# Kernel tuning notes

Hardware: AMD Instinct MI355X
Metric: run time of the kernel (lower is better)

The kernel has to match this reference:

```python
import jax, jax.numpy as jnp
import numpy as np

N_NEURONS = 50000   # dense_shape[0]
N_INPUT = 17400     # dense_shape[1] (LGN units)
NNZ = 1_000_000     # number of sparse synapses
B, T = 1, 256       # batch, timesteps
BKG_SPIKE_RATE = 4  # hardcoded in original call()


def setup_inputs() -> dict:
    key = jax.random.key(0)
    k1, k2, k3, k4, k5 = jax.random.split(key, 5)
    rows = jax.random.randint(k1, (NNZ,), 0, N_NEURONS, dtype=jnp.int32)
    cols = jax.random.randint(k2, (NNZ,), 0, N_INPUT, dtype=jnp.int32)
    weights = jax.random.normal(k3, (NNZ,), dtype=jnp.float32)
    bkg_weights = jax.random.normal(k4, (N_NEURONS,), dtype=jnp.float32)
    inp = jax.random.uniform(k5, (B, T, N_INPUT), dtype=jnp.float32)
    return {"inp": inp, "weights": weights, "bkg_weights": bkg_weights,
            "rows": rows, "cols": cols}


def reference(inp, weights, bkg_weights, rows, cols):
    b, t, n_in = inp.shape
    x = inp.reshape(b * t, n_in)                     # (BT, n_input)
    # Sparse COO matmul: current[n, bt] = sum_{k: rows[k]==n} weights[k] * x[bt, cols[k]]
    # Equivalent to tf.sparse.sparse_dense_matmul(W_sparse, x, adjoint_b=True).
    contrib = weights[:, None] * x.T[cols]           # (nnz, BT)
    cur = jax.ops.segment_sum(contrib, rows, num_segments=N_NEURONS)  # (N, BT)
    cur = cur.T                                      # (BT, N) -- tf.transpose
    # Background noise: uniform(0,1) < 1 is always True, so rest == BKG_SPIKE_RATE.
    u = jax.random.uniform(jax.random.key(42), (b, t, BKG_SPIKE_RATE))
    rest = jnp.sum((u < 1.0).astype(inp.dtype), axis=-1)   # (b, t), constant 4
    noise = bkg_weights[None, None, :] * rest[..., None]   # (b, t, N)
    return cur.reshape(b, t, -1) + noise
```

## Files before the change

### kernel.cpp

```cpp
#include <hip/hip_runtime.h>

#define N_NEURONS 50000
#define N_INPUT   17400
#define NNZ_TOTAL 1000000
#define T_STEPS   256
#define ELL_CAP   64

__global__ __launch_bounds__(256) void transpose_kernel(
    const float* __restrict__ inp, ushort* __restrict__ xTb) {
    __shared__ float tile[32][33];
    const int bx = blockIdx.x;
    const int by = blockIdx.y;
    const int tx = threadIdx.x;
    const int ty = threadIdx.y;

    const int c = bx * 32 + tx;
#pragma unroll
    for (int i = 0; i < 4; ++i) {
        const int r = by * 32 + ty + i * 8;
        if (c < N_INPUT)
            tile[ty + i * 8][tx] = inp[r * N_INPUT + c];
    }
    __syncthreads();

    const int t = by * 32 + tx;
#pragma unroll
    for (int i = 0; i < 4; ++i) {
        const int rr = bx * 32 + ty + i * 8;
        if (rr < N_INPUT) {
            unsigned u = __float_as_uint(tile[tx][ty + i * 8]);
            u += 0x7fffu + ((u >> 16) & 1u);
            xTb[(size_t)rr * T_STEPS + t] = (ushort)(u >> 16);
        }
    }
}

__global__ __launch_bounds__(256) void ell_build_kernel(
    const int* __restrict__ rows, const int* __restrict__ cols,
    const float* __restrict__ w, int* __restrict__ cnt,
    float2* __restrict__ ell) {
    const int i = blockIdx.x * blockDim.x + threadIdx.x;
    if (i < NNZ_TOTAL) {
        const int r = rows[i];
        const int p = atomicAdd(&cnt[r], 1);
        if (p < ELL_CAP)
            ell[(size_t)r * ELL_CAP + p] =
                make_float2(w[i], __int_as_float(cols[i]));
    }
}

__global__ __launch_bounds__(256) void spmm_kernel(
    const uint2* __restrict__ xT2,
    const int* __restrict__ cnt, const float2* __restrict__ ell,
    const float* __restrict__ bkg, float* __restrict__ out) {
    __shared__ float lds[16][260];
    const int tid  = threadIdx.x;
    const int lane = tid & 63;
    const int wv   = tid >> 6;
    const int base = blockIdx.x * 16;
    const int n0   = base + wv * 4;

    const int4   cv  = *(const int4*)&cnt[n0];
    const float4 bgv = *(const float4*)&bkg[n0];
    const int cs[4] = {min(cv.x, ELL_CAP), min(cv.y, ELL_CAP),
                       min(cv.z, ELL_CAP), min(cv.w, ELL_CAP)};
    float2 mv[4];
#pragma unroll
    for (int q = 0; q < 4; ++q)
        mv[q] = ell[(size_t)(n0 + q) * ELL_CAP + lane];

#pragma unroll
    for (int q = 0; q < 4; ++q) {
        float4 acc = make_float4(0.f, 0.f, 0.f, 0.f);
        const int c = cs[q];
        for (int k = 0; k < c; ++k) {
            const float wk = __shfl(mv[q].x, k);
            const int   ck = __float_as_int(__shfl(mv[q].y, k));
            const uint2 xv = xT2[(size_t)ck * 64 + lane];
            const float x0 = __uint_as_float((xv.x & 0xffffu) << 16);
            const float x1 = __uint_as_float(xv.x & 0xffff0000u);
            const float x2 = __uint_as_float((xv.y & 0xffffu) << 16);
            const float x3 = __uint_as_float(xv.y & 0xffff0000u);
            acc.x = fmaf(wk, x0, acc.x);
            acc.y = fmaf(wk, x1, acc.y);
            acc.z = fmaf(wk, x2, acc.z);
            acc.w = fmaf(wk, x3, acc.w);
        }
        const float b4 = 4.0f * ((q == 0) ? bgv.x : (q == 1) ? bgv.y
                                : (q == 2) ? bgv.z : bgv.w);
        acc.x += b4; acc.y += b4; acc.z += b4; acc.w += b4;
        *(float4*)&lds[wv * 4 + q][lane * 4] = acc;
    }
    __syncthreads();

    const int c4 = (tid & 3) * 4;
    const int t0 = tid >> 2;
#pragma unroll
    for (int t = t0; t < T_STEPS; t += 64) {
        float4 v;
        v.x = lds[c4 + 0][t];
        v.y = lds[c4 + 1][t];
        v.z = lds[c4 + 2][t];
        v.w = lds[c4 + 3][t];
        *(float4*)&out[(size_t)t * N_NEURONS + base + c4] = v;
    }
}

extern "C" void kernel_launch(void* const* d_in, const int* in_sizes, int n_in,
                              void* d_out, int out_size, void* d_ws,
                              size_t ws_size, hipStream_t stream) {
    const float* inp     = (const float*)d_in[0];
    const float* weights = (const float*)d_in[1];
    const float* bkg     = (const float*)d_in[2];
    const int*   rows    = (const int*)d_in[3];
    const int*   cols    = (const int*)d_in[4];
    float*       out     = (float*)d_out;

    size_t off = 0;
    auto wsalloc = [&](size_t bytes) -> void* {
        void* p = (char*)d_ws + off;
        off += (bytes + 255) & ~size_t(255);
        return p;
    };
    ushort* xTb = (ushort*)wsalloc(sizeof(ushort) * N_INPUT * T_STEPS);
    int*    cnt = (int*)wsalloc(sizeof(int) * N_NEURONS);
    float2* ell = (float2*)wsalloc(sizeof(float2) * N_NEURONS * ELL_CAP);
    (void)ws_size;

    hipMemsetAsync(cnt, 0, sizeof(int) * N_NEURONS, stream);

    transpose_kernel<<<dim3((N_INPUT + 31) / 32, T_STEPS / 32), dim3(32, 8), 0,
                       stream>>>(inp, xTb);

    const int nb = (NNZ_TOTAL + 255) / 256;
    ell_build_kernel<<<nb, 256, 0, stream>>>(rows, cols, weights, cnt, ell);

    spmm_kernel<<<N_NEURONS / 16, 256, 0, stream>>>(
        (const uint2*)xTb, cnt, ell, bkg, out);
}
```

Before: 229.5 us.

## Pack ELL entries into 32-bit words and batch gathers eight at a time

Each ELL entry now fits in one 32-bit word, with the column index in the high 16 bits and a bf16-rounded weight in the low 16 bits. This halves ELL storage and traffic. The SpMM inner loop issues eight independent gathers before doing the FMAs, which gives more memory-level parallelism. The count is rounded up to a multiple of eight, so the padded slots must read as zero; for that the memset now clears the whole ELL buffer, adding about 12.8MB of extra zeroing. Output uses nontemporal stores, and the bf16 weights reduce precision.

Result: faster. 201.4 us (-12.2%).

```diff
diff --git a/kernel.cpp b/kernel.cpp
--- a/kernel.cpp
+++ b/kernel.cpp
@@ -5,6 +5,8 @@
 #define NNZ_TOTAL 1000000
 #define T_STEPS   256
 #define ELL_CAP   64
+
+typedef float f4_t __attribute__((ext_vector_type(4)));
 
 __global__ __launch_bounds__(256) void transpose_kernel(
     const float* __restrict__ inp, ushort* __restrict__ xTb) {
@@ -38,20 +40,23 @@
 __global__ __launch_bounds__(256) void ell_build_kernel(
     const int* __restrict__ rows, const int* __restrict__ cols,
     const float* __restrict__ w, int* __restrict__ cnt,
-    float2* __restrict__ ell) {
+    unsigned* __restrict__ ell) {
     const int i = blockIdx.x * blockDim.x + threadIdx.x;
     if (i < NNZ_TOTAL) {
         const int r = rows[i];
         const int p = atomicAdd(&cnt[r], 1);
-        if (p < ELL_CAP)
+        if (p < ELL_CAP) {
+            unsigned u = __float_as_uint(w[i]);
+            u += 0x7fffu + ((u >> 16) & 1u);
             ell[(size_t)r * ELL_CAP + p] =
-                make_float2(w[i], __int_as_float(cols[i]));
+                ((unsigned)cols[i] << 16) | (u >> 16);
+        }
     }
 }
 
 __global__ __launch_bounds__(256) void spmm_kernel(
     const uint2* __restrict__ xT2,
-    const int* __restrict__ cnt, const float2* __restrict__ ell,
+    const int* __restrict__ cnt, const unsigned* __restrict__ ell,
     const float* __restrict__ bkg, float* __restrict__ out) {
     __shared__ float lds[16][260];
     const int tid  = threadIdx.x;
@@ -62,32 +67,37 @@
 
     const int4   cv  = *(const int4*)&cnt[n0];
     const float4 bgv = *(const float4*)&bkg[n0];
-    const int cs[4] = {min(cv.x, ELL_CAP), min(cv.y, ELL_CAP),
-                       min(cv.z, ELL_CAP), min(cv.w, ELL_CAP)};
-    float2 mv[4];
+    unsigned ev[4];
 #pragma unroll
     for (int q = 0; q < 4; ++q)
-        mv[q] = ell[(size_t)(n0 + q) * ELL_CAP + lane];
+        ev[q] = ell[(size_t)(n0 + q) * ELL_CAP + lane];
 
 #pragma unroll
     for (int q = 0; q < 4; ++q) {
+        const int c = min((q == 0) ? cv.x : (q == 1) ? cv.y
+                          : (q == 2) ? cv.z : cv.w, ELL_CAP);
+        const int cpad = (c + 7) & ~7;
         float4 acc = make_float4(0.f, 0.f, 0.f, 0.f);
-        const int c = cs[q];
-        for (int k = 0; k < c; ++k) {
-            const float wk = __shfl(mv[q].x, k);
-            const int   ck = __float_as_int(__shfl(mv[q].y, k));
-            const uint2 xv = xT2[(size_t)ck * 64 + lane];
-            const float x0 = __uint_as_float((xv.x & 0xffffu) << 16);
-            const float x1 = __uint_as_float(xv.x & 0xffff0000u);
-            const float x2 = __uint_as_float((xv.y & 0xffffu) << 16);
-            const float x3 = __uint_as_float(xv.y & 0xffff0000u);
-            acc.x = fmaf(wk, x0, acc.x);
-            acc.y = fmaf(wk, x1, acc.y);
-            acc.z = fmaf(wk, x2, acc.z);
-            acc.w = fmaf(wk, x3, acc.w);
+
+        for (int k0 = 0; k0 < cpad; k0 += 8) {
+            unsigned e[8];
+            uint2 xv[8];
+#pragma unroll
+            for (int j = 0; j < 8; ++j) e[j] = __shfl(ev[q], k0 + j);
+#pragma unroll
+            for (int j = 0; j < 8; ++j)
+                xv[j] = xT2[(size_t)(e[j] >> 16) * 64 + lane];
+#pragma unroll
+            for (int j = 0; j < 8; ++j) {
+                const float wk = __uint_as_float(e[j] << 16);
+                acc.x = fmaf(wk, __uint_as_float((xv[j].x & 0xffffu) << 16), acc.x);
+                acc.y = fmaf(wk, __uint_as_float(xv[j].x & 0xffff0000u),     acc.y);
+                acc.z = fmaf(wk, __uint_as_float((xv[j].y & 0xffffu) << 16), acc.z);
+                acc.w = fmaf(wk, __uint_as_float(xv[j].y & 0xffff0000u),     acc.w);
+            }
         }
         const float b4 = 4.0f * ((q == 0) ? bgv.x : (q == 1) ? bgv.y
-                                : (q == 2) ? bgv.z : bgv.w);
+                                 : (q == 2) ? bgv.z : bgv.w);
         acc.x += b4; acc.y += b4; acc.z += b4; acc.w += b4;
         *(float4*)&lds[wv * 4 + q][lane * 4] = acc;
     }
@@ -97,12 +107,13 @@
     const int t0 = tid >> 2;
 #pragma unroll
     for (int t = t0; t < T_STEPS; t += 64) {
-        float4 v;
+        f4_t v;
         v.x = lds[c4 + 0][t];
         v.y = lds[c4 + 1][t];
         v.z = lds[c4 + 2][t];
         v.w = lds[c4 + 3][t];
-        *(float4*)&out[(size_t)t * N_NEURONS + base + c4] = v;
+        __builtin_nontemporal_store(
+            v, (f4_t*)&out[(size_t)t * N_NEURONS + base + c4]);
     }
 }
 
@@ -122,12 +133,14 @@
         off += (bytes + 255) & ~size_t(255);
         return p;
     };
-    ushort* xTb = (ushort*)wsalloc(sizeof(ushort) * N_INPUT * T_STEPS);
-    int*    cnt = (int*)wsalloc(sizeof(int) * N_NEURONS);
-    float2* ell = (float2*)wsalloc(sizeof(float2) * N_NEURONS * ELL_CAP);
+    ushort*   xTb = (ushort*)wsalloc(sizeof(ushort) * N_INPUT * T_STEPS);
+    int*      cnt = (int*)wsalloc(sizeof(int) * N_NEURONS);
+    unsigned* ell = (unsigned*)wsalloc(sizeof(unsigned) * N_NEURONS * ELL_CAP);
     (void)ws_size;
 
-    hipMemsetAsync(cnt, 0, sizeof(int) * N_NEURONS, stream);
+    const size_t zlen = ((char*)ell + sizeof(unsigned) * N_NEURONS * ELL_CAP)
+                        - (char*)cnt;
+    (void)hipMemsetAsync(cnt, 0, zlen, stream);
 
     transpose_kernel<<<dim3((N_INPUT + 31) / 32, T_STEPS / 32), dim3(32, 8), 0,
                        stream>>>(inp, xTb);
```
